# Kernel optimization log

Measured on AMD Instinct MI355X. Metric: run time of the kernel, lower is better.

## Reference

```python
import jax, jax.numpy as jnp
import numpy as np

VOCAB, H, HALF = 64, 64, 32
B, L = 256, 2048
LN_EPS = 1e-5


def _normalize(x):
    # F.normalize: x / max(||x||_2, 1e-12)
    n = jnp.linalg.norm(x, axis=-1, keepdims=True)
    return x / jnp.maximum(n, 1e-12)


def setup_inputs() -> dict:
    key = jax.random.key(0)
    ks = jax.random.split(key, 12)
    def lin(k, fin, fout):
        return jax.random.normal(k, (fin, fout), jnp.float32) / np.sqrt(fin)
    return {
        "seq": jax.random.randint(ks[0], (B, L), 0, VOCAB),
        "embed": jax.random.normal(ks[1], (VOCAB, H), jnp.float32) * 0.02,
        "w1": lin(ks[2], H, 2 * H), "b1": jnp.zeros((2 * H,), jnp.float32),
        "w2": lin(ks[3], 2 * H, H), "b2": jnp.zeros((H,), jnp.float32),
        "ln_g": jnp.ones((H,), jnp.float32), "ln_b": jnp.zeros((H,), jnp.float32),
        "ws": lin(ks[4], H, HALF), "bs": jnp.zeros((HALF,), jnp.float32),
        "we": lin(ks[5], H, HALF), "be": jnp.zeros((HALF,), jnp.float32),
        "wrp": lin(ks[6], 2 * HALF, H), "brp": jnp.zeros((H,), jnp.float32),
        "wout": lin(ks[7], H, VOCAB), "bout": jnp.zeros((VOCAB,), jnp.float32),
    }


def reference(seq, embed, w1, b1, w2, b2, ln_g, ln_b, ws, bs, we, be, wrp, brp, wout, bout):
    b, l = seq.shape
    h = embed[seq]  # [B,L,H]
    ff = jax.nn.relu(h @ w1 + b1) @ w2 + b2
    x = h + ff
    mu = jnp.mean(x, axis=-1, keepdims=True)
    var = jnp.mean((x - mu) ** 2, axis=-1, keepdims=True)
    h = (x - mu) * jax.lax.rsqrt(var + LN_EPS) * ln_g + ln_b  # [B,L,H]

    # precompute projections for the L-1 update steps
    hs = h[:, : l - 1] @ ws + bs           # [B,L-1,HALF]
    he = h[:, : l - 1] @ we + be
    k_s = _normalize(hs)
    k_e = _normalize(he)
    coef = (jnp.arange(1, l, dtype=h.dtype) / l)  # (t+1)/L

    def step(carry, inp):
        Ms, Me = carry
        ks_t, ke_t, hs_t, he_t, c = inp
        vps = jnp.einsum('bij,bj->bi', Ms, ks_t)
        vpe = jnp.einsum('bij,bj->bi', Me, ke_t)
        Ms = Ms + (hs_t - vps)[:, :, None] * ks_t[:, None, :]
        Me = Me + c * (he_t - vpe)[:, :, None] * ke_t[:, None, :]
        return (Ms, Me), None

    M0 = jnp.zeros((b, HALF, HALF), h.dtype)
    xs = (jnp.swapaxes(k_s, 0, 1), jnp.swapaxes(k_e, 0, 1),
          jnp.swapaxes(hs, 0, 1), jnp.swapaxes(he, 0, 1), coef)
    (Ms, Me), _ = jax.lax.scan(step, (M0, M0), xs)

    q = h[:, -1, :]
    qs = _normalize(q @ ws + bs)
    qe = _normalize(q @ we + be)
    rs = jnp.einsum('bij,bj->bi', Ms, qs)
    re = jnp.einsum('bij,bj->bi', Me, qe)
    r = jnp.concatenate([rs, re], axis=-1)  # [B,2*HALF]
    return (r @ wrp + brp) @ wout + bout     # [B,VOCAB]
```

## Files before the change

kernel.cpp:

```cpp
#include <hip/hip_runtime.h>
#include <hip/hip_bf16.h>


#define L_SEQ 2048
#define NPOS  2047

__device__ __forceinline__ float rdlane(float v, int l) {
    return __int_as_float(__builtin_amdgcn_readlane(__float_as_int(v), l));
}

__global__ void build_tables(const float* __restrict__ embed,
                             const float* __restrict__ w1, const float* __restrict__ b1,
                             const float* __restrict__ w2, const float* __restrict__ b2,
                             const float* __restrict__ ln_g, const float* __restrict__ ln_b,
                             const float* __restrict__ ws, const float* __restrict__ bs,
                             const float* __restrict__ we, const float* __restrict__ be,
                             float* __restrict__ tabs) {
    const int v = blockIdx.x;
    const int t = threadIdx.x;
    __shared__ float sh_h[64];
    __shared__ float sh_a[128];
    __shared__ float sh_x[64];

    sh_h[t] = embed[v * 64 + t];
    __syncthreads();

    float acc0 = b1[t], acc1 = b1[t + 64];
    #pragma unroll 8
    for (int k = 0; k < 64; ++k) {
        const float hv = sh_h[k];
        acc0 += hv * w1[k * 128 + t];
        acc1 += hv * w1[k * 128 + t + 64];
    }
    sh_a[t]      = fmaxf(acc0, 0.f);
    sh_a[t + 64] = fmaxf(acc1, 0.f);
    __syncthreads();

    float x = sh_h[t] + b2[t];
    #pragma unroll 8
    for (int k = 0; k < 128; ++k) x += sh_a[k] * w2[k * 64 + t];

    float mu = x;
    for (int m = 1; m <= 32; m <<= 1) mu += __shfl_xor(mu, m);
    mu *= (1.f / 64.f);
    const float dx = x - mu;
    float var = dx * dx;
    for (int m = 1; m <= 32; m <<= 1) var += __shfl_xor(var, m);
    var *= (1.f / 64.f);
    const float hln = dx * rsqrtf(var + 1e-5f) * ln_g[t] + ln_b[t];
    sh_x[t] = hln;
    __syncthreads();

    const int j   = t & 31;
    const int mem = t >> 5;
    const float* W  = mem ? we : ws;
    const float* Bv = mem ? be : bs;
    float p = Bv[j];
    #pragma unroll 8
    for (int k = 0; k < 64; ++k) p += sh_x[k] * W[k * 32 + j];

    float nn = p * p;
    for (int m = 1; m <= 16; m <<= 1) nn += __shfl_xor(nn, m);
    const float kn = p / fmaxf(sqrtf(nn), 1e-12f);

    tabs[(mem * 64 + v) * 32 + j]        = kn;
    tabs[4096 + (mem * 64 + v) * 32 + j] = p;
}

__global__ void gram_kernel(const float* __restrict__ tabs, float* __restrict__ gout) {
    const int v  = blockIdx.x;
    const int tt = threadIdx.x;
    const int m  = tt >> 6, w = tt & 63;
    __shared__ float kv[64];
    if (tt < 64) kv[tt] = tabs[((tt >> 5) * 64 + v) * 32 + (tt & 31)];
    __syncthreads();
    const float* kw  = &tabs[(m * 64 + w) * 32];
    const float* kvm = &kv[m * 32];
    float acc = 0.f;
    #pragma unroll 8
    for (int j = 0; j < 32; ++j) acc += kvm[j] * kw[j];
    gout[m * 4096 + v * 64 + w] = acc;
}

__global__ void __launch_bounds__(128, 1) scan_kernel(const int* __restrict__ seq,
                                                      const float* __restrict__ tabs,
                                                      float* __restrict__ rbuf) {
    const int b    = blockIdx.x;
    const int tid  = threadIdx.x;
    const int m    = tid >> 6;
    const int lane = tid & 63;
    const int q    = lane & 31;

    __shared__ float gt [2 * 64 * 65];
    __shared__ float hsh[2 * 64 * 32];

    for (int i = tid; i < 8192; i += 128) {
        const int mm = i >> 12, v = (i >> 6) & 63, ww = i & 63;
        gt[mm * 4160 + v * 65 + ww] = tabs[16384 + i];
    }
    for (int i = tid; i < 1024; i += 128)
        ((float4*)hsh)[i] = ((const float4*)(tabs + 4096))[i];
    __syncthreads();

    const int*  srow  = seq + b * L_SEQ;
    const int   rowV  = m * 4160 + lane * 65;
    const float invL  = 1.0f / (float)L_SEQ;
    const bool  mF    = (m != 0);
    const float invLe = mF ? invL : 0.0f;

    const int tokL = srow[NPOS];
    float gf = gt[rowV + tokL];
    float W  = 0.f;

    {
        int tk[31]; float cg[31];
        #pragma unroll
        for (int j = 0; j < 31; ++j) tk[j] = srow[2016 + j];
        #pragma unroll
        for (int j = 0; j < 31; ++j) cg[j] = gt[rowV + tk[j]];
        __builtin_amdgcn_sched_barrier(0);
        const float cb = mF ? (float)(2016 + 1) * invL : 1.0f;
        #pragma unroll
        for (int j = 30; j >= 0; --j) {
            const float d = rdlane(gf, tk[j]);
            const float c = cb + (float)j * invLe;
            const float e = c * d;
            gf = fmaf(-e, cg[j], gf);
            W += (lane == tk[j]) ? e : 0.f;
        }
    }

    for (int pb = 1984; pb >= 0; pb -= 32) {
        if (__all(fabsf(gf) < 1e-6f)) break;

        int tk[32]; float cg[32];
        #pragma unroll
        for (int j = 0; j < 32; ++j) tk[j] = srow[pb + j];
        #pragma unroll
        for (int j = 0; j < 32; ++j) cg[j] = gt[rowV + tk[j]];
        __builtin_amdgcn_sched_barrier(0);

        const float cb = mF ? (float)(pb + 1) * invL : 1.0f;
        #pragma unroll
        for (int j = 31; j >= 0; --j) {
            const float d = rdlane(gf, tk[j]);
            const float c = cb + (float)j * invLe;
            const float e = c * d;
            gf = fmaf(-e, cg[j], gf);
            W += (lane == tk[j]) ? e : 0.f;
        }
    }

    float r = 0.f;
    #pragma unroll 8
    for (int v = 0; v < 64; ++v) {
        const float wv = rdlane(W, v);
        r = fmaf(wv, hsh[(m * 64 + v) * 32 + q], r);
    }

    if (lane < 32)
        rbuf[b * 64 + m * 32 + q] = r;
}

__global__ void out_kernel(const float* __restrict__ rbuf,
                           const float* __restrict__ wrp, const float* __restrict__ brp,
                           const float* __restrict__ wout, const float* __restrict__ bout,
                           float* __restrict__ out) {
    const int b = blockIdx.x;
    const int t = threadIdx.x;
    __shared__ float rsh[64];
    __shared__ float ysh[64];

    rsh[t] = rbuf[b * 64 + t];
    __syncthreads();

    float y = brp[t];
    #pragma unroll 8
    for (int k = 0; k < 64; ++k) y += rsh[k] * wrp[k * 64 + t];
    ysh[t] = y;
    __syncthreads();

    float o = bout[t];
    #pragma unroll 8
    for (int k = 0; k < 64; ++k) o += ysh[k] * wout[k * 64 + t];
    out[b * 64 + t] = o;
}

extern "C" void kernel_launch(void* const* d_in, const int* in_sizes, int n_in,
                              void* d_out, int out_size, void* d_ws, size_t ws_size,
                              hipStream_t stream) {
    const int*   seq   = (const int*)  d_in[0];
    const float* embed = (const float*)d_in[1];
    const float* w1    = (const float*)d_in[2];
    const float* b1    = (const float*)d_in[3];
    const float* w2    = (const float*)d_in[4];
    const float* b2    = (const float*)d_in[5];
    const float* ln_g  = (const float*)d_in[6];
    const float* ln_b  = (const float*)d_in[7];
    const float* ws    = (const float*)d_in[8];
    const float* bs    = (const float*)d_in[9];
    const float* we    = (const float*)d_in[10];
    const float* be    = (const float*)d_in[11];
    const float* wrp   = (const float*)d_in[12];
    const float* brp   = (const float*)d_in[13];
    const float* wout  = (const float*)d_in[14];
    const float* bout  = (const float*)d_in[15];

    float* tabs = (float*)d_ws;
    float* gout = tabs + 16384;
    float* rbuf = tabs + 24576;

    build_tables<<<64, 64, 0, stream>>>(embed, w1, b1, w2, b2, ln_g, ln_b,
                                        ws, bs, we, be, tabs);
    gram_kernel<<<64, 128, 0, stream>>>(tabs, gout);
    scan_kernel<<<256, 128, 0, stream>>>(seq, tabs, rbuf);
    out_kernel<<<256, 64, 0, stream>>>(rbuf, wrp, brp, wout, bout, (float*)d_out);
}
```

Measured before the change: 73.42 us.

## Pair reverse-scan steps via precomputed cross-Gram terms to shorten dependency chain

The backward Gram-based scan now processes two timesteps per iteration: both broadcast values come from gf before either update, and the lower step's value is corrected with a precomputed cross term G[tk_low][tk_high] fetched by ds_bpermute. This halves the serial readlane→fma dependency chain. Broadcasts switch from readlane (scalar) to ds_bpermute (LDS crossbar), which has higher latency but lets the two lookups issue independently. The early-exit threshold is loosened from 1e-6 to 1e-4, which may cut the loop short sooner at some accuracy risk, and the ragged first block is folded in by zeroing its last coefficient.

```diff
diff --git a/kernel.cpp b/kernel.cpp
--- a/kernel.cpp
+++ b/kernel.cpp
@@ -7,6 +7,9 @@
 
 __device__ __forceinline__ float rdlane(float v, int l) {
     return __int_as_float(__builtin_amdgcn_readlane(__float_as_int(v), l));
+}
+__device__ __forceinline__ float bperm(int byteaddr, float v) {
+    return __int_as_float(__builtin_amdgcn_ds_bpermute(byteaddr, __float_as_int(v)));
 }
 
 __global__ void build_tables(const float* __restrict__ embed,
@@ -112,42 +115,42 @@
     float gf = gt[rowV + tokL];
     float W  = 0.f;
 
-    {
-        int tk[31]; float cg[31];
-        #pragma unroll
-        for (int j = 0; j < 31; ++j) tk[j] = srow[2016 + j];
-        #pragma unroll
-        for (int j = 0; j < 31; ++j) cg[j] = gt[rowV + tk[j]];
+    for (int pb = 2016; pb >= 0; pb -= 32) {
+        if (__all(fabsf(gf) < 1e-4f)) break;
+
+        int tk[32];
+        #pragma unroll
+        for (int j = 0; j < 32; ++j) tk[j] = srow[pb + j];
+
+        float cg[32];
+        #pragma unroll
+        for (int j = 0; j < 32; ++j) cg[j] = gt[rowV + tk[j]];
+
+        float ga[16];
+        #pragma unroll
+        for (int k = 0; k < 16; ++k)
+            ga[k] = bperm(tk[2*k] << 2, cg[2*k + 1]);
+
+        const float cb = mF ? (float)(pb + 1) * invL : 1.0f;
+        float cc[32];
+        #pragma unroll
+        for (int j = 0; j < 32; ++j) cc[j] = cb + (float)j * invLe;
+        if (pb == 2016) cc[31] = 0.f;
+
         __builtin_amdgcn_sched_barrier(0);
-        const float cb = mF ? (float)(2016 + 1) * invL : 1.0f;
-        #pragma unroll
-        for (int j = 30; j >= 0; --j) {
-            const float d = rdlane(gf, tk[j]);
-            const float c = cb + (float)j * invLe;
-            const float e = c * d;
-            gf = fmaf(-e, cg[j], gf);
-            W += (lane == tk[j]) ? e : 0.f;
-        }
-    }
-
-    for (int pb = 1984; pb >= 0; pb -= 32) {
-        if (__all(fabsf(gf) < 1e-6f)) break;
-
-        int tk[32]; float cg[32];
-        #pragma unroll
-        for (int j = 0; j < 32; ++j) tk[j] = srow[pb + j];
-        #pragma unroll
-        for (int j = 0; j < 32; ++j) cg[j] = gt[rowV + tk[j]];
-        __builtin_amdgcn_sched_barrier(0);
-
-        const float cb = mF ? (float)(pb + 1) * invL : 1.0f;
-        #pragma unroll
-        for (int j = 31; j >= 0; --j) {
-            const float d = rdlane(gf, tk[j]);
-            const float c = cb + (float)j * invLe;
-            const float e = c * d;
-            gf = fmaf(-e, cg[j], gf);
-            W += (lane == tk[j]) ? e : 0.f;
+
+        #pragma unroll
+        for (int k = 15; k >= 0; --k) {
+            const int jh = 2*k + 1, jl = 2*k;
+            const float bh = bperm(tk[jh] << 2, gf);
+            const float bl = bperm(tk[jl] << 2, gf);
+            const float eh = cc[jh] * bh;
+            const float dl = fmaf(-ga[k], eh, bl);
+            const float el = cc[jl] * dl;
+            gf = fmaf(-eh, cg[jh], gf);
+            gf = fmaf(-el, cg[jl], gf);
+            W += (lane == tk[jh]) ? eh : 0.f;
+            W += (lane == tk[jl]) ? el : 0.f;
         }
     }
 
```

New measurement: 99.31 us. 1.35x slower.
